# Kernel optimization log

Measured on AMD Instinct MI355X. Metric: run time of the kernel, lower is better.

Reference implementation:

```python
import jax, jax.numpy as jnp
import numpy as np

B, N, E, F, U = 256, 240, 4338, 28, 100
NEG_SLOPE = 0.2  # PyG GATConv default negative_slope


def setup_inputs() -> dict:
    key = jax.random.key(0)
    ks = jax.random.split(key, 13)
    s = 0.05  # xavier-ish scale
    return {
        "inputs": jax.random.normal(ks[0], (B, N * F), jnp.float32),
        "state": jax.random.normal(ks[1], (B, N * U), jnp.float32),
        "edge_src": jax.random.randint(ks[2], (E,), 0, N, jnp.int32),
        "edge_dst": jax.random.randint(ks[3], (E,), 0, N, jnp.int32),
        # GATConv(U+F -> U): linear weight, attention vectors, output bias
        "Wg": jax.random.normal(ks[4], (U, U + F), jnp.float32) * s,
        "att_src": jax.random.normal(ks[5], (U,), jnp.float32) * s,
        "att_dst": jax.random.normal(ks[6], (U,), jnp.float32) * s,
        "gat_bias": jnp.zeros((U,), jnp.float32),
        # bias_1 added in _gc3 (self.biases[(100,)])
        "bias1": jnp.zeros((U,), jnp.float32),
        # GRU1: GRULinear(100, 200); GRU2: GRULinear(100, 100)
        "W_ru": jax.random.normal(ks[7], (U + F, 2 * U), jnp.float32) * s,
        "b_ru": jnp.zeros((2 * U,), jnp.float32),
        "W_c": jax.random.normal(ks[8], (U + F, U), jnp.float32) * s,
        "b_c": jnp.zeros((U,), jnp.float32),
    }


def _gat_gru(inputs, state, src, dst, Wg, att_src, att_dst, gat_bias, bias1,
             W_ru, b_ru, W_c, b_c):
    xi = inputs.reshape(B, N, F)
    xs = state.reshape(B, N, U)
    # _gc3: concat [state, inputs] -> GATConv per sample (vectorized here)
    x = jnp.concatenate([xs, xi], axis=2)                 # [B, N, U+F]
    h = jnp.einsum("bnf,cf->bnc", x, Wg)                  # [B, N, U]
    a_src = h @ att_src                                    # [B, N]
    a_dst = h @ att_dst                                    # [B, N]
    e = jax.nn.leaky_relu(a_src[:, src] + a_dst[:, dst], NEG_SLOPE)  # [B, E+N]
    eT = e.T                                               # [E+N, B]
    emax = jax.ops.segment_max(eT, dst, num_segments=N)    # [N, B]
    ex = jnp.exp(eT - emax[dst])
    denom = jax.ops.segment_sum(ex, dst, num_segments=N)   # [N, B]
    alpha = ex / denom[dst]                                # [E+N, B]
    msgs = h[:, src].transpose(1, 0, 2) * alpha[:, :, None]  # [E+N, B, U]
    agg = jax.ops.segment_sum(msgs, dst, num_segments=N)   # [N, B, U]
    gstate = agg.transpose(1, 0, 2) + gat_bias + bias1     # [B, N, U]
    st = gstate.reshape(B, N * U)
    # GRU gates (GRULinear concatenates [inputs, hidden] on feature dim)
    cat1 = jnp.concatenate([xi, gstate], axis=2).reshape(-1, U + F)
    ru = jax.nn.sigmoid((cat1 @ W_ru + b_ru).reshape(B, N, 2 * U))
    r = ru[..., :U].reshape(B, N * U)
    u = ru[..., U:].reshape(B, N * U)
    cat2 = jnp.concatenate([xi, (r * st).reshape(B, N, U)], axis=2).reshape(-1, U + F)
    c = jnp.tanh(cat2 @ W_c + b_c).reshape(B, N * U)
    return u * st + (1.0 - u) * c


def reference(inputs, state, edge_src, edge_dst, Wg, att_src, att_dst,
              gat_bias, bias1, W_ru, b_ru, W_c, b_c):
    # PyG GATConv default add_self_loops=True
    loops = jnp.arange(N, dtype=edge_src.dtype)
    src = jnp.concatenate([edge_src, loops])
    dst = jnp.concatenate([edge_dst, loops])
    return _gat_gru(inputs, state, src, dst, Wg, att_src, att_dst, gat_bias,
                    bias1, W_ru, b_ru, W_c, b_c)
```

## Files before the change

### kernel.cpp

```cpp
#include <hip/hip_runtime.h>

#define Bb 256
#define Nn 240
#define Ee 4338
#define Ff 28
#define Uu 100
#define Kk 128
#define Mrows (Bb * Nn)
#define ET (Ee + Nn)
#define AS 136

typedef __attribute__((ext_vector_type(8))) short bf16x8;
typedef __attribute__((ext_vector_type(4))) float f32x4;
typedef unsigned short u16;

__device__ __forceinline__ float bf2f(u16 u) {
  union { unsigned int i; float f; } v; v.i = ((unsigned int)u) << 16; return v.f;
}
__device__ __forceinline__ u16 f2bf(float f) {
  union { float ff; unsigned int i; } v; v.ff = f;
  unsigned int x = v.i;
  return (u16)((x + 0x7fffu + ((x >> 16) & 1u)) >> 16);
}
__device__ __forceinline__ void split4(const float4 v, ushort4& h, ushort4& l) {
  u16 h0 = f2bf(v.x), h1 = f2bf(v.y), h2 = f2bf(v.z), h3 = f2bf(v.w);
  h.x = h0; h.y = h1; h.z = h2; h.w = h3;
  l.x = f2bf(v.x - bf2f(h0)); l.y = f2bf(v.y - bf2f(h1));
  l.z = f2bf(v.z - bf2f(h2)); l.w = f2bf(v.w - bf2f(h3));
}

__global__ __launch_bounds__(256) void k_prep(
    const float* __restrict__ Wg, const float* __restrict__ Wru, const float* __restrict__ Wc,
    u16* __restrict__ wgh, u16* __restrict__ wgl,
    u16* __restrict__ wruh, u16* __restrict__ wrul,
    u16* __restrict__ wch, u16* __restrict__ wcl) {
  int gt = blockIdx.x * 256 + threadIdx.x, GS = gridDim.x * 256;
  for (int i = gt; i < 128 * Kk; i += GS) {
    int c = i >> 7, k = i & 127;
    float v = (c < Uu) ? Wg[c * Kk + k] : 0.f;
    u16 h = f2bf(v); wgh[i] = h; wgl[i] = f2bf(v - bf2f(h));
  }
  for (int i = gt; i < 256 * Kk; i += GS) {
    int n = i >> 7, kp = i & 127;
    int k = (kp < Uu) ? (kp + Ff) : (kp - Uu);
    float v = (n < 2 * Uu) ? Wru[k * (2 * Uu) + n] : 0.f;
    u16 h = f2bf(v); wruh[i] = h; wrul[i] = f2bf(v - bf2f(h));
  }
  for (int i = gt; i < 128 * Kk; i += GS) {
    int n = i >> 7, kp = i & 127;
    int k = (kp < Uu) ? (kp + Ff) : (kp - Uu);
    float v = (n < Uu) ? Wc[k * Uu + n] : 0.f;
    u16 h = f2bf(v); wch[i] = h; wcl[i] = f2bf(v - bf2f(h));
  }
}

__global__ __launch_bounds__(256) void k_csr(
    const int* __restrict__ esrc, const int* __restrict__ edst,
    int* __restrict__ coff, int* __restrict__ cslot) {
  __shared__ int cnt[Nn];
  __shared__ int offs[Nn + 1];
  __shared__ int cur[Nn];
  int tid = threadIdx.x;
  for (int n = tid; n < Nn; n += 256) cnt[n] = 0;
  __syncthreads();
  for (int e = tid; e < Ee; e += 256) atomicAdd(&cnt[edst[e]], 1);
  __syncthreads();
  if (tid == 0) {
    int run = 0;
    for (int n = 0; n < Nn; ++n) { offs[n] = run; run += cnt[n] + 1; }
    offs[Nn] = run;
  }
  __syncthreads();
  for (int n = tid; n < Nn; n += 256) cur[n] = offs[n];
  for (int n = tid; n <= Nn; n += 256) coff[n] = offs[n];
  __syncthreads();
  for (int e = tid; e < Ee; e += 256) {
    int d = edst[e];
    cslot[atomicAdd(&cur[d], 1)] = esrc[e];
  }
  for (int n = tid; n < Nn; n += 256) cslot[atomicAdd(&cur[n], 1)] = n;
}

__global__ __launch_bounds__(256, 4) void k_gemm1(
    const float* __restrict__ stt, const float* __restrict__ inp,
    const u16* __restrict__ wgh, const u16* __restrict__ wgl,
    const float* __restrict__ att_s, const float* __restrict__ att_d,
    float* __restrict__ h, float* __restrict__ asrc, float* __restrict__ adst) {
  __shared__ u16 ahL[32 * AS];
  __shared__ u16 alL[32 * AS];
  __shared__ float sredA[32], sredD[32];
  int tid = threadIdx.x;
  int m0 = blockIdx.x * 32;
  if (tid < 32) sredA[tid] = 0.f;
  else if (tid < 64) sredD[tid - 32] = 0.f;
  for (int j = tid; j < 32 * 32; j += 256) {
    int r = j >> 5, g = j & 31;
    float4 v = (g < 25) ? *(const float4*)(stt + (size_t)(m0 + r) * Uu + g * 4)
                        : *(const float4*)(inp + (size_t)(m0 + r) * Ff + (g - 25) * 4);
    ushort4 hh, ll;
    split4(v, hh, ll);
    *(ushort4*)(ahL + r * AS + g * 4) = hh;
    *(ushort4*)(alL + r * AS + g * 4) = ll;
  }
  __syncthreads();

  int w = tid >> 6, l = tid & 63, l15 = l & 15, q = l >> 4;
  f32x4 zero = {0.f, 0.f, 0.f, 0.f};
  float sa[8] = {0.f, 0.f, 0.f, 0.f, 0.f, 0.f, 0.f, 0.f};
  float sd[8] = {0.f, 0.f, 0.f, 0.f, 0.f, 0.f, 0.f, 0.f};

#pragma unroll
  for (int pass = 0; pass < 2; ++pass) {
    int T = pass * 4 + w;
    bf16x8 wh[4], wl[4];
#pragma unroll
    for (int s = 0; s < 4; ++s) {
      const int o = (T * 16 + l15) * Kk + s * 32 + q * 8;
      wh[s] = *(const bf16x8*)(wgh + o);
      wl[s] = *(const bf16x8*)(wgl + o);
    }
    f32x4 acc[2];
    acc[0] = zero; acc[1] = zero;
#pragma unroll
    for (int rt = 0; rt < 2; ++rt) {
#pragma unroll
      for (int s = 0; s < 4; ++s) {
        bf16x8 a = *(const bf16x8*)(ahL + (rt * 16 + l15) * AS + s * 32 + q * 8);
        bf16x8 b = *(const bf16x8*)(alL + (rt * 16 + l15) * AS + s * 32 + q * 8);
        acc[rt] = __builtin_amdgcn_mfma_f32_16x16x32_bf16(a, wh[s], acc[rt], 0, 0, 0);
        acc[rt] = __builtin_amdgcn_mfma_f32_16x16x32_bf16(b, wh[s], acc[rt], 0, 0, 0);
        acc[rt] = __builtin_amdgcn_mfma_f32_16x16x32_bf16(a, wl[s], acc[rt], 0, 0, 0);
      }
    }
    int c = T * 16 + l15;
    float av = (c < Uu) ? att_s[c] : 0.f, dv = (c < Uu) ? att_d[c] : 0.f;
#pragma unroll
    for (int rt = 0; rt < 2; ++rt) {
#pragma unroll
      for (int i = 0; i < 4; ++i) {
        float v = acc[rt][i];
        int row = rt * 16 + q * 4 + i;
        if (c < Uu) h[(size_t)(m0 + row) * Uu + c] = v;
        sa[rt * 4 + i] += v * av;
        sd[rt * 4 + i] += v * dv;
      }
    }
  }
#pragma unroll
  for (int rt = 0; rt < 2; ++rt) {
#pragma unroll
    for (int i = 0; i < 4; ++i) {
      float va = sa[rt * 4 + i], vd = sd[rt * 4 + i];
#pragma unroll
      for (int msk = 1; msk < 16; msk <<= 1) {
        va += __shfl_xor(va, msk, 64);
        vd += __shfl_xor(vd, msk, 64);
      }
      int row = rt * 16 + q * 4 + i;
      if (l15 == 0) {
        atomicAdd(&sredA[row], va);
        atomicAdd(&sredD[row], vd);
      }
    }
  }
  __syncthreads();
  if (tid < 32) {
    asrc[m0 + tid] = sredA[tid];
    adst[m0 + tid] = sredD[tid];
  }
}

__global__ __launch_bounds__(256) void k_attn(
    const int* __restrict__ coff, const int* __restrict__ cslot,
    const float* __restrict__ asrc, const float* __restrict__ adst,
    const float* __restrict__ h, const float* __restrict__ gbias, const float* __restrict__ b1,
    float* __restrict__ gsf) {
  int b = blockIdx.x;
  int w = threadIdx.x >> 6, lane = threadIdx.x & 63;
  int n = blockIdx.y * 4 + w;
  int o0 = coff[n], deg = coff[n + 1] - o0;
  float ad = adst[b * Nn + n];
  const float* hb = h + (size_t)b * Nn * Uu;
  int half = lane >> 5, ll = lane & 31;
  bool act = (ll < 25);

  float ax = 0.f, ay = 0.f, az = 0.f, aw = 0.f;
  float den = 0.f;
  for (int c0 = 0; c0 < deg; c0 += 64) {
    int e = c0 + lane;
    float we = 0.f; int s = 0;
    if (e < deg) {
      s = cslot[o0 + e];
      float sc = asrc[b * Nn + s] + ad;
      sc = (sc > 0.f) ? sc : 0.2f * sc;
      we = __expf(sc);
    }
    float d = we;
#pragma unroll
    for (int msk = 1; msk < 64; msk <<= 1) d += __shfl_xor(d, msk, 64);
    den += d;

    int cn = (deg - c0 < 64) ? (deg - c0) : 64;
    for (int e2 = 0; e2 < cn; e2 += 2) {
      int eh = e2 + half;
      float w2 = __shfl(we, eh, 64);
      int s2 = __shfl(s, eh, 64);
      if (act && eh < cn) {
        const float4 hv = *(const float4*)(hb + (size_t)s2 * Uu + ll * 4);
        ax += w2 * hv.x; ay += w2 * hv.y; az += w2 * hv.z; aw += w2 * hv.w;
      }
    }
  }
  ax += __shfl_xor(ax, 32, 64);
  ay += __shfl_xor(ay, 32, 64);
  az += __shfl_xor(az, 32, 64);
  aw += __shfl_xor(aw, 32, 64);
  if (lane < 25) {
    float inv = 1.f / den;
    int u0 = lane * 4;
    float4 o;
    o.x = ax * inv + gbias[u0 + 0] + b1[u0 + 0];
    o.y = ay * inv + gbias[u0 + 1] + b1[u0 + 1];
    o.z = az * inv + gbias[u0 + 2] + b1[u0 + 2];
    o.w = aw * inv + gbias[u0 + 3] + b1[u0 + 3];
    *(float4*)(gsf + ((size_t)b * Nn + n) * Uu + u0) = o;
  }
}

__global__ __launch_bounds__(256, 4) void k_gru(
    const float* __restrict__ gsf, const float* __restrict__ inp,
    const u16* __restrict__ wruh, const u16* __restrict__ wrul,
    const float* __restrict__ bru,
    const u16* __restrict__ wch, const u16* __restrict__ wcl,
    const float* __restrict__ bc,
    float* __restrict__ out) {
  __shared__ u16 ahL[32 * AS];
  __shared__ u16 alL[32 * AS];
  __shared__ u16 ugQ[32 * Uu];
  int tid = threadIdx.x;
  int m0 = blockIdx.x * 32;
  for (int j = tid; j < 32 * 32; j += 256) {
    int r = j >> 5, g = j & 31;
    float4 v = (g < 25) ? *(const float4*)(gsf + (size_t)(m0 + r) * Uu + g * 4)
                        : *(const float4*)(inp + (size_t)(m0 + r) * Ff + (g - 25) * 4);
    ushort4 hh, ll;
    split4(v, hh, ll);
    *(ushort4*)(ahL + r * AS + g * 4) = hh;
    *(ushort4*)(alL + r * AS + g * 4) = ll;
  }

  int w = tid >> 6, l = tid & 63, l15 = l & 15, q = l >> 4;
  int c0p = w * 16 + l15, c1p = (w + 4) * 16 + l15;

  float sv[2][2][4];
#pragma unroll
  for (int rt = 0; rt < 2; ++rt) {
#pragma unroll
    for (int i = 0; i < 4; ++i) {
      int row = rt * 16 + q * 4 + i;
#pragma unroll
      for (int t = 0; t < 2; ++t) {
        int c = t ? c1p : c0p;
        sv[t][rt][i] = (c < Uu) ? gsf[(size_t)(m0 + row) * Uu + c] : 0.f;
      }
    }
  }
  __syncthreads();

  f32x4 zero = {0.f, 0.f, 0.f, 0.f};
  float pr[2][2][4];

#pragma unroll
  for (int pass = 0; pass < 4; ++pass) {
    int T = pass * 4 + w;
    bf16x8 wh[4], wl[4];
#pragma unroll
    for (int s = 0; s < 4; ++s) {
      const int o = (T * 16 + l15) * Kk + s * 32 + q * 8;
      wh[s] = *(const bf16x8*)(wruh + o);
      wl[s] = *(const bf16x8*)(wrul + o);
    }
    f32x4 acc[2];
    acc[0] = zero; acc[1] = zero;
#pragma unroll
    for (int rt = 0; rt < 2; ++rt) {
#pragma unroll
      for (int s = 0; s < 4; ++s) {
        bf16x8 a = *(const bf16x8*)(ahL + (rt * 16 + l15) * AS + s * 32 + q * 8);
        bf16x8 b = *(const bf16x8*)(alL + (rt * 16 + l15) * AS + s * 32 + q * 8);
        acc[rt] = __builtin_amdgcn_mfma_f32_16x16x32_bf16(a, wh[s], acc[rt], 0, 0, 0);
        acc[rt] = __builtin_amdgcn_mfma_f32_16x16x32_bf16(b, wh[s], acc[rt], 0, 0, 0);
        acc[rt] = __builtin_amdgcn_mfma_f32_16x16x32_bf16(a, wl[s], acc[rt], 0, 0, 0);
      }
    }
    int c = T * 16 + l15;
    float bv = (c < 2 * Uu) ? bru[c] : 0.f;
#pragma unroll
    for (int rt = 0; rt < 2; ++rt) {
#pragma unroll
      for (int i = 0; i < 4; ++i) {
        int row = rt * 16 + q * 4 + i;
        float y = acc[rt][i] + bv;
        float g = 1.f / (1.f + __expf(-y));
        if (pass < 2) {
          if (c < Uu) pr[pass][rt][i] = g * sv[pass][rt][i];
        }
        if (c >= Uu && c < 2 * Uu) {
          ugQ[row * Uu + (c - Uu)] = (u16)(g * 65535.f + 0.5f);
        }
      }
    }
  }

  __syncthreads();
#pragma unroll
  for (int rt = 0; rt < 2; ++rt) {
#pragma unroll
    for (int i = 0; i < 4; ++i) {
      int row = rt * 16 + q * 4 + i;
#pragma unroll
      for (int t = 0; t < 2; ++t) {
        int c = t ? c1p : c0p;
        if (c < Uu) {
          float p = pr[t][rt][i];
          u16 hh = f2bf(p);
          ahL[row * AS + c] = hh;
          alL[row * AS + c] = f2bf(p - bf2f(hh));
        }
      }
    }
  }
  __syncthreads();

#pragma unroll
  for (int t = 0; t < 2; ++t) {
    int T = t * 4 + w;
    bf16x8 wh[4], wl[4];
#pragma unroll
    for (int s = 0; s < 4; ++s) {
      const int o = (T * 16 + l15) * Kk + s * 32 + q * 8;
      wh[s] = *(const bf16x8*)(wch + o);
      wl[s] = *(const bf16x8*)(wcl + o);
    }
    f32x4 acc[2];
    acc[0] = zero; acc[1] = zero;
#pragma unroll
    for (int rt = 0; rt < 2; ++rt) {
#pragma unroll
      for (int s = 0; s < 4; ++s) {
        bf16x8 a = *(const bf16x8*)(ahL + (rt * 16 + l15) * AS + s * 32 + q * 8);
        bf16x8 b = *(const bf16x8*)(alL + (rt * 16 + l15) * AS + s * 32 + q * 8);
        acc[rt] = __builtin_amdgcn_mfma_f32_16x16x32_bf16(a, wh[s], acc[rt], 0, 0, 0);
        acc[rt] = __builtin_amdgcn_mfma_f32_16x16x32_bf16(b, wh[s], acc[rt], 0, 0, 0);
        acc[rt] = __builtin_amdgcn_mfma_f32_16x16x32_bf16(a, wl[s], acc[rt], 0, 0, 0);
      }
    }
    int c = t ? c1p : c0p;
    float bv = (c < Uu) ? bc[c] : 0.f;
#pragma unroll
    for (int rt = 0; rt < 2; ++rt) {
#pragma unroll
      for (int i = 0; i < 4; ++i) {
        int row = rt * 16 + q * 4 + i;
        size_t m = (size_t)(m0 + row);
        if (c < Uu) {
          float y = acc[rt][i] + bv;
          float cv = 1.f - 2.f / (__expf(2.f * y) + 1.f);
          float u = (float)ugQ[row * Uu + c] * (1.f / 65535.f);
          out[m * Uu + c] = u * sv[t][rt][i] + (1.f - u) * cv;
        }
      }
    }
  }
}

extern "C" void kernel_launch(void* const* d_in, const int* in_sizes, int n_in,
                              void* d_out, int out_size, void* d_ws, size_t ws_size,
                              hipStream_t stream) {
  const float* inp   = (const float*)d_in[0];
  const float* stt   = (const float*)d_in[1];
  const int*   esrc  = (const int*)d_in[2];
  const int*   edst  = (const int*)d_in[3];
  const float* Wg    = (const float*)d_in[4];
  const float* att_s = (const float*)d_in[5];
  const float* att_d = (const float*)d_in[6];
  const float* gbias = (const float*)d_in[7];
  const float* b1    = (const float*)d_in[8];
  const float* Wru   = (const float*)d_in[9];
  const float* bru   = (const float*)d_in[10];
  const float* Wc    = (const float*)d_in[11];
  const float* bc    = (const float*)d_in[12];
  float* out = (float*)d_out;

  char* base = (char*)d_ws;
  size_t o = 0;
  auto alloc = [&](size_t bytes) -> void* {
    void* p = base + o;
    o = (o + bytes + 255) & ~(size_t)255;
    return p;
  };
  u16* wgh  = (u16*)alloc(128 * Kk * sizeof(u16));
  u16* wgl  = (u16*)alloc(128 * Kk * sizeof(u16));
  u16* wruh = (u16*)alloc(256 * Kk * sizeof(u16));
  u16* wrul = (u16*)alloc(256 * Kk * sizeof(u16));
  u16* wch  = (u16*)alloc(128 * Kk * sizeof(u16));
  u16* wcl  = (u16*)alloc(128 * Kk * sizeof(u16));
  int* coff  = (int*)alloc((Nn + 1) * sizeof(int));
  int* cslot = (int*)alloc(ET * sizeof(int));
  float* h    = (float*)alloc((size_t)Mrows * Uu * sizeof(float));
  float* asrc = (float*)alloc((size_t)Mrows * sizeof(float));
  float* adst = (float*)alloc((size_t)Mrows * sizeof(float));
  float* gsf  = (float*)alloc((size_t)Mrows * Uu * sizeof(float));

  k_prep<<<32, 256, 0, stream>>>(Wg, Wru, Wc, wgh, wgl, wruh, wrul, wch, wcl);
  k_csr<<<1, 256, 0, stream>>>(esrc, edst, coff, cslot);
  k_gemm1<<<Mrows / 32, 256, 0, stream>>>(stt, inp, wgh, wgl, att_s, att_d, h, asrc, adst);
  k_attn<<<dim3(Bb, 60), 256, 0, stream>>>(coff, cslot, asrc, adst, h, gbias, b1, gsf);
  k_gru<<<Mrows / 32, 256, 0, stream>>>(gsf, inp, wruh, wrul, bru, wch, wcl, bc, out);
}
```

Before: 241.8 us.

## Fuse GAT projection and attention aggregation into one per-sample kernel with LDS-resident h

Replaces the separate projection GEMM and attention kernels with a single kernel that runs one 512-thread block per batch sample. The block computes h for all 240 nodes into shared memory in 16-row chunks, double-buffering the input staging, and accumulates the attention logits in LDS. It then does the softmax-weighted neighbour gather from LDS instead of global memory. This removes the global round trip for h, asrc and adst and one kernel launch, at the cost of about 96KB of LDS per block, only 256 blocks, and a serialized per-chunk GEMM loop that limits occupancy.

```diff
diff --git a/kernel.cpp b/kernel.cpp
--- a/kernel.cpp
+++ b/kernel.cpp
@@ -81,149 +81,133 @@
   for (int n = tid; n < Nn; n += 256) cslot[atomicAdd(&cur[n], 1)] = n;
 }
 
-__global__ __launch_bounds__(256, 4) void k_gemm1(
+__global__ __launch_bounds__(512) void k_ga(
     const float* __restrict__ stt, const float* __restrict__ inp,
     const u16* __restrict__ wgh, const u16* __restrict__ wgl,
     const float* __restrict__ att_s, const float* __restrict__ att_d,
-    float* __restrict__ h, float* __restrict__ asrc, float* __restrict__ adst) {
-  __shared__ u16 ahL[32 * AS];
-  __shared__ u16 alL[32 * AS];
-  __shared__ float sredA[32], sredD[32];
+    const int* __restrict__ coff, const int* __restrict__ cslot,
+    const float* __restrict__ gbias, const float* __restrict__ b1,
+    float* __restrict__ gsf) {
+  __shared__ float hL[Nn * Uu];
+  __shared__ u16 xh[2][16 * AS];
+  __shared__ u16 xl[2][16 * AS];
+  __shared__ float asrcL[Nn], adstL[Nn];
+  int b = blockIdx.x;
   int tid = threadIdx.x;
-  int m0 = blockIdx.x * 32;
-  if (tid < 32) sredA[tid] = 0.f;
-  else if (tid < 64) sredD[tid - 32] = 0.f;
-  for (int j = tid; j < 32 * 32; j += 256) {
-    int r = j >> 5, g = j & 31;
-    float4 v = (g < 25) ? *(const float4*)(stt + (size_t)(m0 + r) * Uu + g * 4)
-                        : *(const float4*)(inp + (size_t)(m0 + r) * Ff + (g - 25) * 4);
+  size_t mb = (size_t)b * Nn;
+
+  for (int i = tid; i < Nn; i += 512) { asrcL[i] = 0.f; adstL[i] = 0.f; }
+
+  int sr = tid >> 5, sg = tid & 31;
+  {
+    size_t m = mb + sr;
+    float4 v = (sg < 25) ? *(const float4*)(stt + m * Uu + sg * 4)
+                         : *(const float4*)(inp + m * Ff + (sg - 25) * 4);
     ushort4 hh, ll;
     split4(v, hh, ll);
-    *(ushort4*)(ahL + r * AS + g * 4) = hh;
-    *(ushort4*)(alL + r * AS + g * 4) = ll;
-  }
-  __syncthreads();
+    *(ushort4*)(&xh[0][sr * AS + sg * 4]) = hh;
+    *(ushort4*)(&xl[0][sr * AS + sg * 4]) = ll;
+  }
 
   int w = tid >> 6, l = tid & 63, l15 = l & 15, q = l >> 4;
+  int c = w * 16 + l15;
+  float av = (c < Uu) ? att_s[c] : 0.f;
+  float dv = (c < Uu) ? att_d[c] : 0.f;
+  bf16x8 wh[4], wl[4];
+#pragma unroll
+  for (int s = 0; s < 4; ++s) {
+    const int o = (w * 16 + l15) * Kk + s * 32 + q * 8;
+    wh[s] = *(const bf16x8*)(wgh + o);
+    wl[s] = *(const bf16x8*)(wgl + o);
+  }
   f32x4 zero = {0.f, 0.f, 0.f, 0.f};
-  float sa[8] = {0.f, 0.f, 0.f, 0.f, 0.f, 0.f, 0.f, 0.f};
-  float sd[8] = {0.f, 0.f, 0.f, 0.f, 0.f, 0.f, 0.f, 0.f};
-
-#pragma unroll
-  for (int pass = 0; pass < 2; ++pass) {
-    int T = pass * 4 + w;
-    bf16x8 wh[4], wl[4];
+  __syncthreads();
+
+  for (int ch = 0; ch < 15; ++ch) {
+    int cur = ch & 1;
+    if (ch + 1 < 15) {
+      size_t m = mb + (ch + 1) * 16 + sr;
+      float4 v = (sg < 25) ? *(const float4*)(stt + m * Uu + sg * 4)
+                           : *(const float4*)(inp + m * Ff + (sg - 25) * 4);
+      ushort4 hh, ll;
+      split4(v, hh, ll);
+      *(ushort4*)(&xh[cur ^ 1][sr * AS + sg * 4]) = hh;
+      *(ushort4*)(&xl[cur ^ 1][sr * AS + sg * 4]) = ll;
+    }
+    f32x4 acc = zero;
 #pragma unroll
     for (int s = 0; s < 4; ++s) {
-      const int o = (T * 16 + l15) * Kk + s * 32 + q * 8;
-      wh[s] = *(const bf16x8*)(wgh + o);
-      wl[s] = *(const bf16x8*)(wgl + o);
-    }
-    f32x4 acc[2];
-    acc[0] = zero; acc[1] = zero;
-#pragma unroll
-    for (int rt = 0; rt < 2; ++rt) {
-#pragma unroll
-      for (int s = 0; s < 4; ++s) {
-        bf16x8 a = *(const bf16x8*)(ahL + (rt * 16 + l15) * AS + s * 32 + q * 8);
-        bf16x8 b = *(const bf16x8*)(alL + (rt * 16 + l15) * AS + s * 32 + q * 8);
-        acc[rt] = __builtin_amdgcn_mfma_f32_16x16x32_bf16(a, wh[s], acc[rt], 0, 0, 0);
-        acc[rt] = __builtin_amdgcn_mfma_f32_16x16x32_bf16(b, wh[s], acc[rt], 0, 0, 0);
-        acc[rt] = __builtin_amdgcn_mfma_f32_16x16x32_bf16(a, wl[s], acc[rt], 0, 0, 0);
-      }
-    }
-    int c = T * 16 + l15;
-    float av = (c < Uu) ? att_s[c] : 0.f, dv = (c < Uu) ? att_d[c] : 0.f;
-#pragma unroll
-    for (int rt = 0; rt < 2; ++rt) {
-#pragma unroll
-      for (int i = 0; i < 4; ++i) {
-        float v = acc[rt][i];
-        int row = rt * 16 + q * 4 + i;
-        if (c < Uu) h[(size_t)(m0 + row) * Uu + c] = v;
-        sa[rt * 4 + i] += v * av;
-        sd[rt * 4 + i] += v * dv;
-      }
-    }
-  }
-#pragma unroll
-  for (int rt = 0; rt < 2; ++rt) {
+      bf16x8 a = *(const bf16x8*)(&xh[cur][l15 * AS + s * 32 + q * 8]);
+      bf16x8 bb = *(const bf16x8*)(&xl[cur][l15 * AS + s * 32 + q * 8]);
+      acc = __builtin_amdgcn_mfma_f32_16x16x32_bf16(a, wh[s], acc, 0, 0, 0);
+      acc = __builtin_amdgcn_mfma_f32_16x16x32_bf16(bb, wh[s], acc, 0, 0, 0);
+      acc = __builtin_amdgcn_mfma_f32_16x16x32_bf16(a, wl[s], acc, 0, 0, 0);
+    }
 #pragma unroll
     for (int i = 0; i < 4; ++i) {
-      float va = sa[rt * 4 + i], vd = sd[rt * 4 + i];
+      float v = acc[i];
+      int n = ch * 16 + q * 4 + i;
+      if (c < Uu) hL[n * Uu + c] = v;
+      float va = v * av, vd = v * dv;
 #pragma unroll
       for (int msk = 1; msk < 16; msk <<= 1) {
         va += __shfl_xor(va, msk, 64);
         vd += __shfl_xor(vd, msk, 64);
       }
-      int row = rt * 16 + q * 4 + i;
       if (l15 == 0) {
-        atomicAdd(&sredA[row], va);
-        atomicAdd(&sredD[row], vd);
-      }
-    }
-  }
-  __syncthreads();
-  if (tid < 32) {
-    asrc[m0 + tid] = sredA[tid];
-    adst[m0 + tid] = sredD[tid];
-  }
-}
-
-__global__ __launch_bounds__(256) void k_attn(
-    const int* __restrict__ coff, const int* __restrict__ cslot,
-    const float* __restrict__ asrc, const float* __restrict__ adst,
-    const float* __restrict__ h, const float* __restrict__ gbias, const float* __restrict__ b1,
-    float* __restrict__ gsf) {
-  int b = blockIdx.x;
-  int w = threadIdx.x >> 6, lane = threadIdx.x & 63;
-  int n = blockIdx.y * 4 + w;
-  int o0 = coff[n], deg = coff[n + 1] - o0;
-  float ad = adst[b * Nn + n];
-  const float* hb = h + (size_t)b * Nn * Uu;
-  int half = lane >> 5, ll = lane & 31;
+        atomicAdd(&asrcL[n], va);
+        atomicAdd(&adstL[n], vd);
+      }
+    }
+    __syncthreads();
+  }
+
+  int half = l >> 5, ll = l & 31;
   bool act = (ll < 25);
-
-  float ax = 0.f, ay = 0.f, az = 0.f, aw = 0.f;
-  float den = 0.f;
-  for (int c0 = 0; c0 < deg; c0 += 64) {
-    int e = c0 + lane;
-    float we = 0.f; int s = 0;
-    if (e < deg) {
-      s = cslot[o0 + e];
-      float sc = asrc[b * Nn + s] + ad;
-      sc = (sc > 0.f) ? sc : 0.2f * sc;
-      we = __expf(sc);
-    }
-    float d = we;
-#pragma unroll
-    for (int msk = 1; msk < 64; msk <<= 1) d += __shfl_xor(d, msk, 64);
-    den += d;
-
-    int cn = (deg - c0 < 64) ? (deg - c0) : 64;
-    for (int e2 = 0; e2 < cn; e2 += 2) {
-      int eh = e2 + half;
-      float w2 = __shfl(we, eh, 64);
-      int s2 = __shfl(s, eh, 64);
-      if (act && eh < cn) {
-        const float4 hv = *(const float4*)(hb + (size_t)s2 * Uu + ll * 4);
-        ax += w2 * hv.x; ay += w2 * hv.y; az += w2 * hv.z; aw += w2 * hv.w;
-      }
-    }
-  }
-  ax += __shfl_xor(ax, 32, 64);
-  ay += __shfl_xor(ay, 32, 64);
-  az += __shfl_xor(az, 32, 64);
-  aw += __shfl_xor(aw, 32, 64);
-  if (lane < 25) {
-    float inv = 1.f / den;
-    int u0 = lane * 4;
-    float4 o;
-    o.x = ax * inv + gbias[u0 + 0] + b1[u0 + 0];
-    o.y = ay * inv + gbias[u0 + 1] + b1[u0 + 1];
-    o.z = az * inv + gbias[u0 + 2] + b1[u0 + 2];
-    o.w = aw * inv + gbias[u0 + 3] + b1[u0 + 3];
-    *(float4*)(gsf + ((size_t)b * Nn + n) * Uu + u0) = o;
+  for (int n = w; n < Nn; n += 8) {
+    int o0 = coff[n], deg = coff[n + 1] - o0;
+    float ad = adstL[n];
+    float ax = 0.f, ay = 0.f, az = 0.f, aw2 = 0.f;
+    float den = 0.f;
+    for (int c0 = 0; c0 < deg; c0 += 64) {
+      int e = c0 + l;
+      float we = 0.f; int s = 0;
+      if (e < deg) {
+        s = cslot[o0 + e];
+        float sc = asrcL[s] + ad;
+        sc = (sc > 0.f) ? sc : 0.2f * sc;
+        we = __expf(sc);
+      }
+      float d = we;
+#pragma unroll
+      for (int msk = 1; msk < 64; msk <<= 1) d += __shfl_xor(d, msk, 64);
+      den += d;
+
+      int cn = (deg - c0 < 64) ? (deg - c0) : 64;
+      for (int e2 = 0; e2 < cn; e2 += 2) {
+        int eh = e2 + half;
+        float w2 = __shfl(we, eh, 64);
+        int s2 = __shfl(s, eh, 64);
+        if (act && eh < cn) {
+          const float4 hv = *(const float4*)(hL + s2 * Uu + ll * 4);
+          ax += w2 * hv.x; ay += w2 * hv.y; az += w2 * hv.z; aw2 += w2 * hv.w;
+        }
+      }
+    }
+    ax += __shfl_xor(ax, 32, 64);
+    ay += __shfl_xor(ay, 32, 64);
+    az += __shfl_xor(az, 32, 64);
+    aw2 += __shfl_xor(aw2, 32, 64);
+    if (l < 25) {
+      float inv = 1.f / den;
+      int u0 = l * 4;
+      float4 o;
+      o.x = ax * inv + gbias[u0 + 0] + b1[u0 + 0];
+      o.y = ay * inv + gbias[u0 + 1] + b1[u0 + 1];
+      o.z = az * inv + gbias[u0 + 2] + b1[u0 + 2];
+      o.w = aw2 * inv + gbias[u0 + 3] + b1[u0 + 3];
+      *(float4*)(gsf + (mb + n) * Uu + u0) = o;
+    }
   }
 }
 
@@ -407,14 +391,11 @@
   u16* wcl  = (u16*)alloc(128 * Kk * sizeof(u16));
   int* coff  = (int*)alloc((Nn + 1) * sizeof(int));
   int* cslot = (int*)alloc(ET * sizeof(int));
-  float* h    = (float*)alloc((size_t)Mrows * Uu * sizeof(float));
-  float* asrc = (float*)alloc((size_t)Mrows * sizeof(float));
-  float* adst = (float*)alloc((size_t)Mrows * sizeof(float));
   float* gsf  = (float*)alloc((size_t)Mrows * Uu * sizeof(float));
 
   k_prep<<<32, 256, 0, stream>>>(Wg, Wru, Wc, wgh, wgl, wruh, wrul, wch, wcl);
   k_csr<<<1, 256, 0, stream>>>(esrc, edst, coff, cslot);
-  k_gemm1<<<Mrows / 32, 256, 0, stream>>>(stt, inp, wgh, wgl, att_s, att_d, h, asrc, adst);
-  k_attn<<<dim3(Bb, 60), 256, 0, stream>>>(coff, cslot, asrc, adst, h, gbias, b1, gsf);
+  k_ga<<<Bb, 512, 0, stream>>>(stt, inp, wgh, wgl, att_s, att_d, coff, cslot,
+                               gbias, b1, gsf);
   k_gru<<<Mrows / 32, 256, 0, stream>>>(gsf, inp, wruh, wrul, bru, wch, wcl, bc, out);
 }
```

Result: slower. 250.6 us (+3.6%).
